# Kernel optimization log

Hardware: AMD Instinct MI355X
Metric: run time of the kernel (lower is better)

The kernel has to match this reference:

```python
import jax, jax.numpy as jnp
import numpy as np

B, S, D_IN, D_OUT = 4, 2048, 2048, 2048
E, R = 8, 8
SCALING = 16.0 / 8.0  # lora_alpha / r
# Dropout (p=0.05) treated as identity (eval mode) for a deterministic reference.

def setup_inputs() -> dict:
    key = jax.random.key(0)
    ks = jax.random.split(key, 8)
    x = jax.random.normal(ks[0], (B, S, D_IN), dtype=jnp.float32)
    base_W = jax.random.normal(ks[1], (D_OUT, D_IN), dtype=jnp.float32) * 0.02
    base_b = jax.random.normal(ks[2], (D_OUT,), dtype=jnp.float32) * 0.02
    shared_A = jax.random.normal(ks[3], (R, D_IN), dtype=jnp.float32) * 0.01
    shared_B = jax.random.normal(ks[4], (D_OUT, R), dtype=jnp.float32) * 0.01
    expert_A = jax.random.normal(ks[5], (E, R, D_IN), dtype=jnp.float32) * 0.01
    expert_B = jax.random.normal(ks[6], (E, D_OUT, R), dtype=jnp.float32) * 0.01
    task_emb = jax.random.normal(ks[7], (E, D_IN), dtype=jnp.float32) * 0.01
    collab_w = jnp.array(0.5, dtype=jnp.float32)
    return {"x": x, "base_W": base_W, "base_b": base_b,
            "shared_A": shared_A, "shared_B": shared_B,
            "expert_A": expert_A, "expert_B": expert_B,
            "task_emb": task_emb, "collab_w": collab_w}

def reference(x, base_W, base_b, shared_A, shared_B, expert_A, expert_B, task_emb, collab_w):
    # base linear: [B,S,D_out]
    base_out = jnp.einsum('bsi,oi->bso', x, base_W) + base_b
    # shared LoRA path
    shared_out = jnp.einsum('bsr,or->bso', jnp.einsum('bsi,ri->bsr', x, shared_A), shared_B) * SCALING
    # soft routing over task experts (task_id=None branch)
    x_mean = x.mean(axis=1)                               # [B,D_in]
    routing = jax.nn.softmax(x_mean @ task_emb.T, axis=-1)  # [B,E]
    t = jnp.einsum('bsi,eri->bser', x, expert_A)          # [B,S,E,R] low-rank
    task_out = jnp.einsum('bser,eor,be->bso', t, expert_B, routing) * SCALING
    cw = jax.nn.sigmoid(collab_w)
    return base_out + cw * shared_out + (1.0 - cw) * task_out
```

## Files before the change

### kernel.cpp

```cpp
#include <hip/hip_runtime.h>
#include <hip/hip_bf16.h>
#include <math.h>

#define BATCH 4
#define SEQ   2048
#define DIN   2048
#define DOUT  2048
#define NEXP  8
#define RANK  8
#define MTOT  (BATCH * SEQ)
#define KP    128

typedef __bf16 bf16x8 __attribute__((ext_vector_type(8)));
typedef __bf16 bf16x4 __attribute__((ext_vector_type(4)));
typedef float  f32x4  __attribute__((ext_vector_type(4)));

#define GLOBAL_AS __attribute__((address_space(1)))
#define LDS_AS    __attribute__((address_space(3)))

__global__ __launch_bounds__(256) void prep_all(
    const float* __restrict__ x, const float* __restrict__ W,
    const float* __restrict__ expert_A, const float* __restrict__ shared_A,
    const float* __restrict__ expert_B, const float* __restrict__ shared_B,
    const float* __restrict__ collab,
    __bf16* __restrict__ xb, float* __restrict__ partial,
    __bf16* __restrict__ Wb, __bf16* __restrict__ caug, __bf16* __restrict__ Ab)
{
    const int bid = blockIdx.x;
    const int t = threadIdx.x;
    if (bid < 256) {
        const int dc = bid & 1, sc = (bid >> 1) & 31, b = bid >> 6;
        const int i = dc * 1024 + t * 4;
        size_t base = ((size_t)b * SEQ + (size_t)sc * 64) * DIN + i;
        float ax = 0.f, ay = 0.f, az = 0.f, aw = 0.f;
        for (int s = 0; s < 64; ++s) {
            float4 v = *(const float4*)&x[base + (size_t)s * DIN];
            ax += v.x; ay += v.y; az += v.z; aw += v.w;
            bf16x4 h = { (__bf16)v.x, (__bf16)v.y, (__bf16)v.z, (__bf16)v.w };
            *(bf16x4*)&xb[base + (size_t)s * DIN] = h;
        }
        float4 p = { ax, ay, az, aw };
        *(float4*)&partial[((size_t)b * 32 + sc) * DIN + i] = p;
    } else if (bid < 4352) {
        size_t idx = ((size_t)(bid - 256) * 256 + t) * 4;
        float4 v = *(const float4*)&W[idx];
        bf16x4 h = { (__bf16)v.x, (__bf16)v.y, (__bf16)v.z, (__bf16)v.w };
        *(bf16x4*)&Wb[idx] = h;
    } else if (bid < 5376) {
        int idx = (bid - 4352) * 256 + t;
        int k = idx & 127, o = idx >> 7;
        float cw = 1.0f / (1.0f + expf(-collab[0]));
        float v = 0.f;
        if (k < 64)
            v = (1.0f - cw) * 2.0f * expert_B[((size_t)(k >> 3) * DOUT + o) * RANK + (k & 7)];
        else if (k < 72)
            v = cw * 2.0f * shared_B[(size_t)o * RANK + (k - 64)];
        caug[idx] = (__bf16)v;
    } else {
        int idx = (bid - 5376) * 256 + t;
        int i = idx & 2047, k = idx >> 11;
        float v = 0.f;
        if (k < 64)      v = expert_A[(size_t)k * DIN + i];
        else if (k < 72) v = shared_A[(size_t)(k - 64) * DIN + i];
        Ab[idx] = (__bf16)v;
    }
}

__global__ __launch_bounds__(256) void gemm_t64(
    const __bf16* __restrict__ xb, const __bf16* __restrict__ Ab,
    const float* __restrict__ partial, const float* __restrict__ task_emb,
    __bf16* __restrict__ tb)
{
    __shared__ __bf16 lsA[128 * 32];
    __shared__ __bf16 lsB[128 * 32];
    __shared__ float red[256];
    __shared__ float rs[NEXP];
    const int t = threadIdx.x;
    const int m0 = blockIdx.x * 128;
    const int b  = m0 >> 11;

    float xm[8] = {0.f,0.f,0.f,0.f,0.f,0.f,0.f,0.f};
    for (int sc = 0; sc < 32; ++sc) {
        const float* pp = partial + ((size_t)b * 32 + sc) * DIN + t * 8;
        float4 v0 = *(const float4*)pp, v1 = *(const float4*)(pp + 4);
        xm[0] += v0.x; xm[1] += v0.y; xm[2] += v0.z; xm[3] += v0.w;
        xm[4] += v1.x; xm[5] += v1.y; xm[6] += v1.z; xm[7] += v1.w;
    }
    float le[NEXP];
    #pragma unroll
    for (int e = 0; e < NEXP; ++e) {
        const float* te = task_emb + (size_t)e * DIN + t * 8;
        float4 u0 = *(const float4*)te, u1 = *(const float4*)(te + 4);
        le[e] = xm[0]*u0.x + xm[1]*u0.y + xm[2]*u0.z + xm[3]*u0.w
              + xm[4]*u1.x + xm[5]*u1.y + xm[6]*u1.z + xm[7]*u1.w;
    }
    for (int e = 0; e < NEXP; ++e) {
        red[t] = le[e];
        __syncthreads();
        for (int s = 128; s > 0; s >>= 1) {
            if (t < s) red[t] += red[t + s];
            __syncthreads();
        }
        if (t == 0) rs[e] = red[0] * (1.0f / (float)SEQ);
        __syncthreads();
    }
    if (t == 0) {
        float mx = rs[0];
        for (int e = 1; e < NEXP; ++e) mx = fmaxf(mx, rs[e]);
        float ex[NEXP], den = 0.f;
        for (int e = 0; e < NEXP; ++e) { ex[e] = expf(rs[e] - mx); den += ex[e]; }
        for (int e = 0; e < NEXP; ++e) rs[e] = ex[e] / den;
    }

    const int lane = t & 63;
    const int wm = (t >> 6) >> 1, wn = (t >> 6) & 1;
    f32x4 acc[4][4];
    #pragma unroll
    for (int a = 0; a < 4; ++a)
        #pragma unroll
        for (int c = 0; c < 4; ++c) acc[a][c] = (f32x4){0.f, 0.f, 0.f, 0.f};

    for (int k0 = 0; k0 < DIN; k0 += 32) {
        #pragma unroll
        for (int q = 0; q < 2; ++q) {
            int L = q * 256 + t;
            int row = L >> 2, seg = L & 3;
            const __bf16* gpA = xb + (size_t)(m0 + row) * DIN + k0 + seg * 8;
            const __bf16* gpB = Ab + (size_t)row * DIN + k0 + seg * 8;
            int Lu = q * 256 + (t & ~63);
            __builtin_amdgcn_global_load_lds((GLOBAL_AS void*)gpA,
                (LDS_AS void*)&lsA[Lu * 8], 16, 0, 0);
            __builtin_amdgcn_global_load_lds((GLOBAL_AS void*)gpB,
                (LDS_AS void*)&lsB[Lu * 8], 16, 0, 0);
        }
        __syncthreads();
        bf16x8 af[4], bfr[4];
        #pragma unroll
        for (int tm = 0; tm < 4; ++tm)
            af[tm]  = *(const bf16x8*)&lsA[(wm * 64 + tm * 16 + (lane & 15)) * 32 + (lane >> 4) * 8];
        #pragma unroll
        for (int tn = 0; tn < 4; ++tn)
            bfr[tn] = *(const bf16x8*)&lsB[(wn * 64 + tn * 16 + (lane & 15)) * 32 + (lane >> 4) * 8];
        #pragma unroll
        for (int tm = 0; tm < 4; ++tm)
            #pragma unroll
            for (int tn = 0; tn < 4; ++tn)
                acc[tm][tn] = __builtin_amdgcn_mfma_f32_16x16x32_bf16(
                    af[tm], bfr[tn], acc[tm][tn], 0, 0, 0);
        __syncthreads();
    }

    #pragma unroll
    for (int tm = 0; tm < 4; ++tm)
        #pragma unroll
        for (int tn = 0; tn < 4; ++tn) {
            int col = wn * 64 + tn * 16 + (lane & 15);
            float f = (col < 64) ? rs[col >> 3] : 1.0f;
            #pragma unroll
            for (int v = 0; v < 4; ++v) {
                int row = m0 + wm * 64 + tm * 16 + (lane >> 4) * 4 + v;
                tb[(size_t)row * KP + col] = (__bf16)(acc[tm][tn][v] * f);
            }
        }
}

__global__ __launch_bounds__(256) void gemm_main(
    const __bf16* __restrict__ xb, const __bf16* __restrict__ Wb,
    const __bf16* __restrict__ tb, const __bf16* __restrict__ caug,
    const float* __restrict__ bias, float* __restrict__ out)
{
    __shared__ __bf16 lsA[128 * 64];
    __shared__ __bf16 lsB[128 * 64];
    const int t = threadIdx.x;
    const int lane = t & 63;
    const int wm = (t >> 6) >> 1, wn = (t >> 6) & 1;
    const int m0 = blockIdx.x * 128;
    const int n0 = blockIdx.y * 128;

    int rowq[4], segq[4], ldso[4];
    #pragma unroll
    for (int q = 0; q < 4; ++q) {
        rowq[q] = q * 32 + (t >> 3);
        segq[q] = (t & 7) ^ (rowq[q] & 7);
        ldso[q] = (q * 256 + (t & ~63)) * 8;
    }
    const __bf16* pA[4]; const __bf16* pB[4];
    #pragma unroll
    for (int q = 0; q < 4; ++q) {
        pA[q] = xb + (size_t)(m0 + rowq[q]) * DIN + segq[q] * 8;
        pB[q] = Wb + (size_t)(n0 + rowq[q]) * DIN + segq[q] * 8;
    }
    int aoff[2][4], boff[2][4];
    #pragma unroll
    for (int tm = 0; tm < 4; ++tm) {
        int r = wm * 64 + tm * 16 + (lane & 15);
        #pragma unroll
        for (int kk = 0; kk < 2; ++kk)
            aoff[kk][tm] = r * 64 + (((kk * 4 + (lane >> 4)) ^ (r & 7)) * 8);
    }
    #pragma unroll
    for (int tn = 0; tn < 4; ++tn) {
        int r = wn * 64 + tn * 16 + (lane & 15);
        #pragma unroll
        for (int kk = 0; kk < 2; ++kk)
            boff[kk][tn] = r * 64 + (((kk * 4 + (lane >> 4)) ^ (r & 7)) * 8);
    }

    f32x4 acc[4][4];
    #pragma unroll
    for (int a = 0; a < 4; ++a)
        #pragma unroll
        for (int c = 0; c < 4; ++c) acc[a][c] = (f32x4){0.f, 0.f, 0.f, 0.f};

    for (int it = 0; it < 32; ++it) {
        #pragma unroll
        for (int q = 0; q < 4; ++q) {
            __builtin_amdgcn_global_load_lds((GLOBAL_AS void*)pA[q],
                (LDS_AS void*)&lsA[ldso[q]], 16, 0, 0);
            __builtin_amdgcn_global_load_lds((GLOBAL_AS void*)pB[q],
                (LDS_AS void*)&lsB[ldso[q]], 16, 0, 0);
            pA[q] += 64; pB[q] += 64;
        }
        __syncthreads();
        #pragma unroll
        for (int kk = 0; kk < 2; ++kk) {
            bf16x8 af[4], bfr[4];
            #pragma unroll
            for (int tm = 0; tm < 4; ++tm) af[tm]  = *(const bf16x8*)&lsA[aoff[kk][tm]];
            #pragma unroll
            for (int tn = 0; tn < 4; ++tn) bfr[tn] = *(const bf16x8*)&lsB[boff[kk][tn]];
            #pragma unroll
            for (int tm = 0; tm < 4; ++tm)
                #pragma unroll
                for (int tn = 0; tn < 4; ++tn)
                    acc[tm][tn] = __builtin_amdgcn_mfma_f32_16x16x32_bf16(
                        af[tm], bfr[tn], acc[tm][tn], 0, 0, 0);
        }
        __syncthreads();
    }

    const __bf16* qA[4]; const __bf16* qB[4];
    #pragma unroll
    for (int q = 0; q < 4; ++q) {
        qA[q] = tb   + (size_t)(m0 + rowq[q]) * KP + segq[q] * 8;
        qB[q] = caug + (size_t)(n0 + rowq[q]) * KP + segq[q] * 8;
    }
    for (int it = 0; it < 2; ++it) {
        #pragma unroll
        for (int q = 0; q < 4; ++q) {
            __builtin_amdgcn_global_load_lds((GLOBAL_AS void*)qA[q],
                (LDS_AS void*)&lsA[ldso[q]], 16, 0, 0);
            __builtin_amdgcn_global_load_lds((GLOBAL_AS void*)qB[q],
                (LDS_AS void*)&lsB[ldso[q]], 16, 0, 0);
            qA[q] += 64; qB[q] += 64;
        }
        __syncthreads();
        #pragma unroll
        for (int kk = 0; kk < 2; ++kk) {
            bf16x8 af[4], bfr[4];
            #pragma unroll
            for (int tm = 0; tm < 4; ++tm) af[tm]  = *(const bf16x8*)&lsA[aoff[kk][tm]];
            #pragma unroll
            for (int tn = 0; tn < 4; ++tn) bfr[tn] = *(const bf16x8*)&lsB[boff[kk][tn]];
            #pragma unroll
            for (int tm = 0; tm < 4; ++tm)
                #pragma unroll
                for (int tn = 0; tn < 4; ++tn)
                    acc[tm][tn] = __builtin_amdgcn_mfma_f32_16x16x32_bf16(
                        af[tm], bfr[tn], acc[tm][tn], 0, 0, 0);
        }
        __syncthreads();
    }

    #pragma unroll
    for (int tm = 0; tm < 4; ++tm)
        #pragma unroll
        for (int tn = 0; tn < 4; ++tn) {
            int col = n0 + wn * 64 + tn * 16 + (lane & 15);
            float bv = bias[col];
            #pragma unroll
            for (int v = 0; v < 4; ++v) {
                int row = m0 + wm * 64 + tm * 16 + (lane >> 4) * 4 + v;
                out[(size_t)row * DOUT + col] = acc[tm][tn][v] + bv;
            }
        }
}

extern "C" void kernel_launch(void* const* d_in, const int* in_sizes, int n_in,
                              void* d_out, int out_size, void* d_ws, size_t ws_size,
                              hipStream_t stream)
{
    const float* x        = (const float*)d_in[0];
    const float* base_W   = (const float*)d_in[1];
    const float* base_b   = (const float*)d_in[2];
    const float* shared_A = (const float*)d_in[3];
    const float* shared_B = (const float*)d_in[4];
    const float* expert_A = (const float*)d_in[5];
    const float* expert_B = (const float*)d_in[6];
    const float* task_emb = (const float*)d_in[7];
    const float* collab_w = (const float*)d_in[8];
    float* out = (float*)d_out;

    char* ws = (char*)d_ws;
    __bf16* xb      = (__bf16*)(ws + 0);
    __bf16* Wb      = (__bf16*)(ws + 33554432);
    __bf16* tb      = (__bf16*)(ws + 41943040);
    __bf16* caug    = (__bf16*)(ws + 44040192);
    __bf16* Ab      = (__bf16*)(ws + 44564480);
    float*  partial = (float*) (ws + 45088768);

    prep_all <<<dim3(6400), 256, 0, stream>>>(x, base_W, expert_A, shared_A,
                                              expert_B, shared_B, collab_w,
                                              xb, partial, Wb, caug, Ab);
    gemm_t64 <<<dim3(64), 256, 0, stream>>>(xb, Ab, partial, task_emb, tb);
    gemm_main<<<dim3(64, 16), 256, 0, stream>>>(xb, Wb, tb, caug, base_b, out);
}
```

Baseline: 260.6 us.

## Fold shared LoRA into base weight and split-K the expert low-rank GEMM

```diff
diff --git a/kernel.cpp b/kernel.cpp
--- a/kernel.cpp
+++ b/kernel.cpp
@@ -9,7 +9,7 @@
 #define NEXP  8
 #define RANK  8
 #define MTOT  (BATCH * SEQ)
-#define KP    128
+#define KE    64
 
 typedef __bf16 bf16x8 __attribute__((ext_vector_type(8)));
 typedef __bf16 bf16x4 __attribute__((ext_vector_type(4)));
@@ -28,140 +28,172 @@
 {
     const int bid = blockIdx.x;
     const int t = threadIdx.x;
-    if (bid < 256) {
-        const int dc = bid & 1, sc = (bid >> 1) & 31, b = bid >> 6;
-        const int i = dc * 1024 + t * 4;
-        size_t base = ((size_t)b * SEQ + (size_t)sc * 64) * DIN + i;
-        float ax = 0.f, ay = 0.f, az = 0.f, aw = 0.f;
-        for (int s = 0; s < 64; ++s) {
-            float4 v = *(const float4*)&x[base + (size_t)s * DIN];
-            ax += v.x; ay += v.y; az += v.z; aw += v.w;
-            bf16x4 h = { (__bf16)v.x, (__bf16)v.y, (__bf16)v.z, (__bf16)v.w };
-            *(bf16x4*)&xb[base + (size_t)s * DIN] = h;
-        }
-        float4 p = { ax, ay, az, aw };
-        *(float4*)&partial[((size_t)b * 32 + sc) * DIN + i] = p;
-    } else if (bid < 4352) {
-        size_t idx = ((size_t)(bid - 256) * 256 + t) * 4;
-        float4 v = *(const float4*)&W[idx];
+    if (bid < 1024) {
+        const int dc = bid & 3, sc = (bid >> 2) & 63, b = bid >> 8;
+        const int i = dc * 512 + t * 2;
+        size_t base = ((size_t)b * SEQ + (size_t)sc * 32) * DIN + i;
+        float a0 = 0.f, a1 = 0.f;
+        for (int s = 0; s < 32; ++s) {
+            float2 v = *(const float2*)&x[base + (size_t)s * DIN];
+            a0 += v.x; a1 += v.y;
+            __bf16 h0 = (__bf16)v.x, h1 = (__bf16)v.y;
+            ((__bf16*)&xb[base + (size_t)s * DIN])[0] = h0;
+            ((__bf16*)&xb[base + (size_t)s * DIN])[1] = h1;
+        }
+        float2 p = { a0, a1 };
+        *(float2*)&partial[((size_t)b * 64 + sc) * DIN + i] = p;
+    } else if (bid < 5120) {
+        int idx = (bid - 1024) * 1024 + t * 4;
+        int o = idx >> 11, i = idx & 2047;
+        float cw = 1.0f / (1.0f + expf(-collab[0]));
+        float s = cw * 2.0f;
+        float4 w = *(const float4*)&W[idx];
+        float dx = 0.f, dy = 0.f, dz = 0.f, dw = 0.f;
+        #pragma unroll
+        for (int r = 0; r < 8; ++r) {
+            float bs = shared_B[(size_t)o * RANK + r];
+            float4 as = *(const float4*)&shared_A[(size_t)r * DIN + i];
+            dx += bs * as.x; dy += bs * as.y; dz += bs * as.z; dw += bs * as.w;
+        }
+        bf16x4 h = { (__bf16)(w.x + s * dx), (__bf16)(w.y + s * dy),
+                     (__bf16)(w.z + s * dz), (__bf16)(w.w + s * dw) };
+        *(bf16x4*)&Wb[idx] = h;
+    } else if (bid < 5632) {
+        int idx = (bid - 5120) * 256 + t;
+        int k = idx & 63, o = idx >> 6;
+        float cw = 1.0f / (1.0f + expf(-collab[0]));
+        caug[idx] = (__bf16)((1.0f - cw) * 2.0f *
+            expert_B[((size_t)(k >> 3) * DOUT + o) * RANK + (k & 7)]);
+    } else {
+        int idx = (bid - 5632) * 1024 + t * 4;
+        float4 v = *(const float4*)&expert_A[idx];
         bf16x4 h = { (__bf16)v.x, (__bf16)v.y, (__bf16)v.z, (__bf16)v.w };
-        *(bf16x4*)&Wb[idx] = h;
-    } else if (bid < 5376) {
-        int idx = (bid - 4352) * 256 + t;
-        int k = idx & 127, o = idx >> 7;
-        float cw = 1.0f / (1.0f + expf(-collab[0]));
-        float v = 0.f;
-        if (k < 64)
-            v = (1.0f - cw) * 2.0f * expert_B[((size_t)(k >> 3) * DOUT + o) * RANK + (k & 7)];
-        else if (k < 72)
-            v = cw * 2.0f * shared_B[(size_t)o * RANK + (k - 64)];
-        caug[idx] = (__bf16)v;
-    } else {
-        int idx = (bid - 5376) * 256 + t;
-        int i = idx & 2047, k = idx >> 11;
-        float v = 0.f;
-        if (k < 64)      v = expert_A[(size_t)k * DIN + i];
-        else if (k < 72) v = shared_A[(size_t)(k - 64) * DIN + i];
-        Ab[idx] = (__bf16)v;
-    }
-}
-
-__global__ __launch_bounds__(256) void gemm_t64(
+        *(bf16x4*)&Ab[idx] = h;
+    }
+}
+
+__global__ __launch_bounds__(256) void gemm_t_rout(
     const __bf16* __restrict__ xb, const __bf16* __restrict__ Ab,
     const float* __restrict__ partial, const float* __restrict__ task_emb,
-    __bf16* __restrict__ tb)
+    __bf16* __restrict__ pt, float* __restrict__ routing)
 {
     __shared__ __bf16 lsA[128 * 32];
-    __shared__ __bf16 lsB[128 * 32];
+    __shared__ __bf16 lsB[64 * 32];
     __shared__ float red[256];
-    __shared__ float rs[NEXP];
+    const int bid = blockIdx.x;
     const int t = threadIdx.x;
-    const int m0 = blockIdx.x * 128;
-    const int b  = m0 >> 11;
-
-    float xm[8] = {0.f,0.f,0.f,0.f,0.f,0.f,0.f,0.f};
-    for (int sc = 0; sc < 32; ++sc) {
-        const float* pp = partial + ((size_t)b * 32 + sc) * DIN + t * 8;
-        float4 v0 = *(const float4*)pp, v1 = *(const float4*)(pp + 4);
-        xm[0] += v0.x; xm[1] += v0.y; xm[2] += v0.z; xm[3] += v0.w;
-        xm[4] += v1.x; xm[5] += v1.y; xm[6] += v1.z; xm[7] += v1.w;
-    }
-    float le[NEXP];
-    #pragma unroll
-    for (int e = 0; e < NEXP; ++e) {
-        const float* te = task_emb + (size_t)e * DIN + t * 8;
-        float4 u0 = *(const float4*)te, u1 = *(const float4*)(te + 4);
-        le[e] = xm[0]*u0.x + xm[1]*u0.y + xm[2]*u0.z + xm[3]*u0.w
-              + xm[4]*u1.x + xm[5]*u1.y + xm[6]*u1.z + xm[7]*u1.w;
-    }
-    for (int e = 0; e < NEXP; ++e) {
-        red[t] = le[e];
-        __syncthreads();
-        for (int s = 128; s > 0; s >>= 1) {
-            if (t < s) red[t] += red[t + s];
+
+    if (bid >= 256) {
+        const int b = bid - 256;
+        float xm[8] = {0.f,0.f,0.f,0.f,0.f,0.f,0.f,0.f};
+        for (int sc = 0; sc < 64; ++sc) {
+            const float* pp = partial + ((size_t)b * 64 + sc) * DIN + t * 8;
+            float4 v0 = *(const float4*)pp, v1 = *(const float4*)(pp + 4);
+            xm[0] += v0.x; xm[1] += v0.y; xm[2] += v0.z; xm[3] += v0.w;
+            xm[4] += v1.x; xm[5] += v1.y; xm[6] += v1.z; xm[7] += v1.w;
+        }
+        float le[NEXP];
+        #pragma unroll
+        for (int e = 0; e < NEXP; ++e) {
+            const float* te = task_emb + (size_t)e * DIN + t * 8;
+            float4 u0 = *(const float4*)te, u1 = *(const float4*)(te + 4);
+            le[e] = xm[0]*u0.x + xm[1]*u0.y + xm[2]*u0.z + xm[3]*u0.w
+                  + xm[4]*u1.x + xm[5]*u1.y + xm[6]*u1.z + xm[7]*u1.w;
+        }
+        __shared__ float logits[NEXP];
+        for (int e = 0; e < NEXP; ++e) {
+            red[t] = le[e];
             __syncthreads();
-        }
-        if (t == 0) rs[e] = red[0] * (1.0f / (float)SEQ);
-        __syncthreads();
-    }
-    if (t == 0) {
-        float mx = rs[0];
-        for (int e = 1; e < NEXP; ++e) mx = fmaxf(mx, rs[e]);
-        float ex[NEXP], den = 0.f;
-        for (int e = 0; e < NEXP; ++e) { ex[e] = expf(rs[e] - mx); den += ex[e]; }
-        for (int e = 0; e < NEXP; ++e) rs[e] = ex[e] / den;
+            for (int s = 128; s > 0; s >>= 1) {
+                if (t < s) red[t] += red[t + s];
+                __syncthreads();
+            }
+            if (t == 0) logits[e] = red[0] * (1.0f / (float)SEQ);
+            __syncthreads();
+        }
+        if (t == 0) {
+            float mx = logits[0];
+            for (int e = 1; e < NEXP; ++e) mx = fmaxf(mx, logits[e]);
+            float ex[NEXP], den = 0.f;
+            for (int e = 0; e < NEXP; ++e) { ex[e] = expf(logits[e] - mx); den += ex[e]; }
+            for (int e = 0; e < NEXP; ++e) routing[b * NEXP + e] = ex[e] / den;
+        }
+        return;
     }
 
     const int lane = t & 63;
-    const int wm = (t >> 6) >> 1, wn = (t >> 6) & 1;
-    f32x4 acc[4][4];
-    #pragma unroll
-    for (int a = 0; a < 4; ++a)
+    const int w = t >> 6;
+    const int kc = bid & 3;
+    const int m0 = (bid >> 2) * 128;
+
+    f32x4 acc[2][4];
+    #pragma unroll
+    for (int a = 0; a < 2; ++a)
         #pragma unroll
         for (int c = 0; c < 4; ++c) acc[a][c] = (f32x4){0.f, 0.f, 0.f, 0.f};
 
-    for (int k0 = 0; k0 < DIN; k0 += 32) {
+    for (int k0 = kc * 512; k0 < kc * 512 + 512; k0 += 32) {
         #pragma unroll
         for (int q = 0; q < 2; ++q) {
             int L = q * 256 + t;
             int row = L >> 2, seg = L & 3;
             const __bf16* gpA = xb + (size_t)(m0 + row) * DIN + k0 + seg * 8;
-            const __bf16* gpB = Ab + (size_t)row * DIN + k0 + seg * 8;
             int Lu = q * 256 + (t & ~63);
             __builtin_amdgcn_global_load_lds((GLOBAL_AS void*)gpA,
                 (LDS_AS void*)&lsA[Lu * 8], 16, 0, 0);
+        }
+        {
+            int row = t >> 2, seg = t & 3;
+            const __bf16* gpB = Ab + (size_t)row * DIN + k0 + seg * 8;
             __builtin_amdgcn_global_load_lds((GLOBAL_AS void*)gpB,
-                (LDS_AS void*)&lsB[Lu * 8], 16, 0, 0);
-        }
-        __syncthreads();
-        bf16x8 af[4], bfr[4];
-        #pragma unroll
-        for (int tm = 0; tm < 4; ++tm)
-            af[tm]  = *(const bf16x8*)&lsA[(wm * 64 + tm * 16 + (lane & 15)) * 32 + (lane >> 4) * 8];
+                (LDS_AS void*)&lsB[(t & ~63) * 8], 16, 0, 0);
+        }
+        __syncthreads();
+        bf16x8 af[2], bfr[4];
+        #pragma unroll
+        for (int tm = 0; tm < 2; ++tm)
+            af[tm] = *(const bf16x8*)&lsA[(w * 32 + tm * 16 + (lane & 15)) * 32 + (lane >> 4) * 8];
         #pragma unroll
         for (int tn = 0; tn < 4; ++tn)
-            bfr[tn] = *(const bf16x8*)&lsB[(wn * 64 + tn * 16 + (lane & 15)) * 32 + (lane >> 4) * 8];
-        #pragma unroll
-        for (int tm = 0; tm < 4; ++tm)
+            bfr[tn] = *(const bf16x8*)&lsB[(tn * 16 + (lane & 15)) * 32 + (lane >> 4) * 8];
+        #pragma unroll
+        for (int tm = 0; tm < 2; ++tm)
             #pragma unroll
             for (int tn = 0; tn < 4; ++tn)
                 acc[tm][tn] = __builtin_amdgcn_mfma_f32_16x16x32_bf16(
                     af[tm], bfr[tn], acc[tm][tn], 0, 0, 0);
         __syncthreads();
     }
-
-    #pragma unroll
-    for (int tm = 0; tm < 4; ++tm)
+    #pragma unroll
+    for (int tm = 0; tm < 2; ++tm)
         #pragma unroll
         for (int tn = 0; tn < 4; ++tn) {
-            int col = wn * 64 + tn * 16 + (lane & 15);
-            float f = (col < 64) ? rs[col >> 3] : 1.0f;
+            int col = tn * 16 + (lane & 15);
             #pragma unroll
             for (int v = 0; v < 4; ++v) {
-                int row = m0 + wm * 64 + tm * 16 + (lane >> 4) * 4 + v;
-                tb[(size_t)row * KP + col] = (__bf16)(acc[tm][tn][v] * f);
+                int row = m0 + w * 32 + tm * 16 + (lane >> 4) * 4 + v;
+                pt[((size_t)kc * MTOT + row) * KE + col] = (__bf16)acc[tm][tn][v];
             }
         }
+}
+
+__global__ __launch_bounds__(256) void reduce_route(
+    const __bf16* __restrict__ pt, const float* __restrict__ routing,
+    __bf16* __restrict__ tb)
+{
+    size_t idx = ((size_t)blockIdx.x * 256 + threadIdx.x) * 4;
+    int k0 = (int)(idx & 63);
+    int m  = (int)(idx >> 6);
+    int b  = m >> 11;
+    float f = routing[b * NEXP + (k0 >> 3)];
+    float sx = 0.f, sy = 0.f, sz = 0.f, sw = 0.f;
+    #pragma unroll
+    for (int kc = 0; kc < 4; ++kc) {
+        bf16x4 v = *(const bf16x4*)&pt[(size_t)kc * MTOT * KE + idx];
+        sx += (float)v[0]; sy += (float)v[1]; sz += (float)v[2]; sw += (float)v[3];
+    }
+    bf16x4 h = { (__bf16)(sx * f), (__bf16)(sy * f), (__bf16)(sz * f), (__bf16)(sw * f) };
+    *(bf16x4*)&tb[idx] = h;
 }
 
 __global__ __launch_bounds__(256) void gemm_main(
@@ -239,20 +271,15 @@
         __syncthreads();
     }
 
-    const __bf16* qA[4]; const __bf16* qB[4];
-    #pragma unroll
-    for (int q = 0; q < 4; ++q) {
-        qA[q] = tb   + (size_t)(m0 + rowq[q]) * KP + segq[q] * 8;
-        qB[q] = caug + (size_t)(n0 + rowq[q]) * KP + segq[q] * 8;
-    }
-    for (int it = 0; it < 2; ++it) {
+    {
         #pragma unroll
         for (int q = 0; q < 4; ++q) {
-            __builtin_amdgcn_global_load_lds((GLOBAL_AS void*)qA[q],
+            const __bf16* qA = tb   + (size_t)(m0 + rowq[q]) * KE + segq[q] * 8;
+            const __bf16* qB = caug + (size_t)(n0 + rowq[q]) * KE + segq[q] * 8;
+            __builtin_amdgcn_global_load_lds((GLOBAL_AS void*)qA,
                 (LDS_AS void*)&lsA[ldso[q]], 16, 0, 0);
-            __builtin_amdgcn_global_load_lds((GLOBAL_AS void*)qB[q],
+            __builtin_amdgcn_global_load_lds((GLOBAL_AS void*)qB,
                 (LDS_AS void*)&lsB[ldso[q]], 16, 0, 0);
-            qA[q] += 64; qB[q] += 64;
         }
         __syncthreads();
         #pragma unroll
@@ -304,14 +331,17 @@
     char* ws = (char*)d_ws;
     __bf16* xb      = (__bf16*)(ws + 0);
     __bf16* Wb      = (__bf16*)(ws + 33554432);
-    __bf16* tb      = (__bf16*)(ws + 41943040);
-    __bf16* caug    = (__bf16*)(ws + 44040192);
-    __bf16* Ab      = (__bf16*)(ws + 44564480);
-    float*  partial = (float*) (ws + 45088768);
-
-    prep_all <<<dim3(6400), 256, 0, stream>>>(x, base_W, expert_A, shared_A,
-                                              expert_B, shared_B, collab_w,
-                                              xb, partial, Wb, caug, Ab);
-    gemm_t64 <<<dim3(64), 256, 0, stream>>>(xb, Ab, partial, task_emb, tb);
-    gemm_main<<<dim3(64, 16), 256, 0, stream>>>(xb, Wb, tb, caug, base_b, out);
-}
+    __bf16* pt      = (__bf16*)(ws + 41943040);
+    __bf16* tb      = (__bf16*)(ws + 46137344);
+    __bf16* caug    = (__bf16*)(ws + 47185920);
+    __bf16* Ab      = (__bf16*)(ws + 47448064);
+    float*  partial = (float*) (ws + 47710208);
+    float*  routing = (float*) (ws + 49807360);
+
+    prep_all    <<<dim3(5760), 256, 0, stream>>>(x, base_W, expert_A, shared_A,
+                                                 expert_B, shared_B, collab_w,
+                                                 xb, partial, Wb, caug, Ab);
+    gemm_t_rout <<<dim3(260), 256, 0, stream>>>(xb, Ab, partial, task_emb, pt, routing);
+    reduce_route<<<dim3(512), 256, 0, stream>>>(pt, routing, tb);
+    gemm_main   <<<dim3(64, 16), 256, 0, stream>>>(xb, Wb, tb, caug, base_b, out);
+}
```

Result: faster. 242.4 us (-7.0%).
